# Kernel optimization log

Measured on AMD Instinct MI355X. Metric: run time of the kernel, lower is better.

## Reference

```python
import jax, jax.numpy as jnp
import numpy as np

B, T, IN_DIM, HID, OUT_DIM = 32, 2000, 118, 256, 118


def sru_layer(x, W, b):
    """One SRU layer. x: [B,T,n_in]; W: [n_in, k*d] with k=3 (n_in==d) or k=4; b: [2*d].
    c_t = f_t*c_{t-1} + (1-f_t)*x~_t ;  h_t = r_t*tanh(c_t) + (1-r_t)*x_hw_t
    """
    d = b.shape[0] // 2
    k = W.shape[1] // d
    U = jnp.einsum('bti,io->bto', x, W)  # [B,T,k*d] gate precompute (GEMM)
    x_tilde = U[..., :d]
    f = jax.nn.sigmoid(U[..., d:2 * d] + b[:d])
    r = jax.nn.sigmoid(U[..., 2 * d:3 * d] + b[d:])
    x_hw = U[..., 3 * d:4 * d] if k == 4 else x  # highway input (projected if dims differ)

    # elementwise recurrent scan over time (time-major)
    def step(c, ft_xt):
        ft, xt = ft_xt
        c = ft * c + (1.0 - ft) * xt
        return c, c

    f_t = jnp.swapaxes(f, 0, 1)        # [T,B,d]
    x_t = jnp.swapaxes(x_tilde, 0, 1)  # [T,B,d]
    c0 = jnp.zeros((x.shape[0], d), dtype=x.dtype)
    _, c_seq = jax.lax.scan(step, c0, (f_t, x_t))
    c = jnp.swapaxes(c_seq, 0, 1)      # [B,T,d]
    return r * jnp.tanh(c) + (1.0 - r) * x_hw


def setup_inputs() -> dict:
    key = jax.random.key(0)
    ks = jax.random.split(key, 8)
    sequence = jax.random.normal(ks[0], (B, T, IN_DIM), dtype=jnp.float32)
    lengths = jax.random.randint(ks[1], (B,), 1, T + 1)
    s0 = 1.0 / np.sqrt(IN_DIM)
    s1 = 1.0 / np.sqrt(HID)
    W0 = jax.random.uniform(ks[2], (IN_DIM, 4 * HID), jnp.float32, -s0, s0)  # k=4: n_in != n_out
    b0 = jnp.zeros((2 * HID,), jnp.float32)
    W1 = jax.random.uniform(ks[3], (HID, 3 * HID), jnp.float32, -s1, s1)    # k=3: n_in == n_out
    b1 = jnp.zeros((2 * HID,), jnp.float32)
    Wout = jax.random.uniform(ks[4], (HID, OUT_DIM), jnp.float32, -s1, s1)
    bout = jax.random.uniform(ks[5], (OUT_DIM,), jnp.float32, -s1, s1)
    return {"sequence": sequence, "lengths": lengths, "W0": W0, "b0": b0,
            "W1": W1, "b1": b1, "Wout": Wout, "bout": bout}


def reference(sequence, lengths, W0, b0, W1, b1, Wout, bout):
    h = sru_layer(sequence, W0, b0)
    h = sru_layer(h, W1, b1)
    out = jnp.einsum('btd,do->bto', h, Wout) + bout  # hidden2out Linear
    return out  # last_sigmoid=False
```

## Files before the change

kernel.cpp:

```cpp
#include <hip/hip_runtime.h>


typedef __attribute__((ext_vector_type(8))) __bf16 bf16x8;
typedef __attribute__((ext_vector_type(4))) float f32x4;
typedef __attribute__((ext_vector_type(4))) unsigned int u32x4;

static __device__ __forceinline__ float fast_sigmoid(float x) {
    float e = __expf(-x);
    return __builtin_amdgcn_rcpf(1.f + e);
}
static __device__ __forceinline__ float fast_tanh(float x) {
    float e = __expf(-2.f * fabsf(x));
    float t = (1.f - e) * __builtin_amdgcn_rcpf(1.f + e);
    return copysignf(t, x);
}
static __device__ __forceinline__ unsigned short f2bf(float f) {
    union { float f; unsigned u; } v; v.f = f;
    return (unsigned short)((v.u + 0x7fffu + ((v.u >> 16) & 1u)) >> 16);
}
static __device__ __forceinline__ float bf2f(unsigned short h) {
    union { unsigned u; float f; } v; v.u = ((unsigned)h) << 16;
    return v.f;
}

static constexpr int T = 2000;

__global__ void prep_x_kernel(const float* __restrict__ x, unsigned short* __restrict__ xp) {
    int i = blockIdx.x * 256 + threadIdx.x;
    if (i >= 64000 * 128) return;
    int row = i >> 7, k = i & 127;
    float v = (k < 118) ? x[row * 118 + k] : 0.f;
    xp[i] = f2bf(v);
}

__global__ void prep_w_kernel(const float* __restrict__ W0, const float* __restrict__ W1,
                              const float* __restrict__ Wout,
                              unsigned short* __restrict__ W0t, unsigned short* __restrict__ W1t,
                              unsigned short* __restrict__ Wot) {
    int i = blockIdx.x * 256 + threadIdx.x;
    if (i < 1024 * 128) {
        int n = i >> 7, k = i & 127;
        float v = (k < 118) ? W0[k * 1024 + n] : 0.f;
        W0t[i] = f2bf(v);
        return;
    }
    i -= 1024 * 128;
    if (i < 768 * 256) {
        int n = i >> 8, k = i & 255;
        W1t[i] = f2bf(W1[k * 768 + n]);
        return;
    }
    i -= 768 * 256;
    if (i < 128 * 256) {
        int n = i >> 8, k = i & 255;
        float v = (n < 118) ? Wout[k * 118 + n] : 0.f;
        Wot[i] = f2bf(v);
    }
}

template <int KP, int KFAC>
__global__ __launch_bounds__(256, 4)
void sru_wave_kernel(const unsigned short* __restrict__ xin,
                     const unsigned short* __restrict__ Wt,
                     const float* __restrict__ bvec,
                     unsigned short* __restrict__ hout) {
    constexpr int KST   = KP / 32;
    constexpr int CPR   = KP / 8;
    constexpr int ROWB  = KP * 2;
    constexpr int CHUNK = 250;
    constexpr int WARM  = 64;

    __shared__ unsigned short sW[KFAC * 16 * KP];

    const int tid   = threadIdx.x;
    const int lane  = tid & 63;
    const int w     = tid >> 6;
    const int slice = blockIdx.x >> 6;
    const int chunk = (blockIdx.x >> 3) & 7;
    const int bgrp  = blockIdx.x & 7;
    const int d0    = slice * 16;
    const int b     = bgrp * 4 + w;

    {
        constexpr int NCHK = KFAC * 16 * CPR;
        for (int i = tid; i < NCHK; i += 256) {
            int row = i / CPR, c = i % CPR;
            int ch = row & 15, gate = row >> 4;
            u32x4 v = *(const u32x4*)(Wt + (size_t)(gate * 256 + d0 + ch) * KP + c * 8);
            *(u32x4*)((char*)sW + row * ROWB + ((c * 16) ^ (ch << 4))) = v;
        }
    }
    __syncthreads();

    const int nl = lane & 15;
    const int q  = lane >> 4;

    const float bf_r = bvec[d0 + nl];
    const float br_r = bvec[256 + d0 + nl];

    const unsigned short* xb = xin + (size_t)b * T * KP;
    unsigned short* hb = hout + (size_t)b * T * 256;

    const int tR = chunk * CHUNK;
    const int tW = chunk ? tR - WARM : 0;
    const int tE = tR + CHUNK;

    float c_in = 0.f;

    for (int t0 = tW; t0 < tE; t0 += 16) {
        int ta = t0 + nl; if (ta > T - 1) ta = T - 1;
        const unsigned short* ap = xb + (size_t)ta * KP + q * 8;

        unsigned short xh[4];
        if constexpr (KFAC == 3) {
#pragma unroll
            for (int j = 0; j < 4; ++j) {
                int t = t0 + q * 4 + j;
                if (t > T - 1) t = T - 1;
                xh[j] = xb[(size_t)t * KP + d0 + nl];
            }
        }

        f32x4 acc[KFAC];
        const f32x4 fz = {0.f, 0.f, 0.f, 0.f};
#pragma unroll
        for (int g = 0; g < KFAC; ++g) acc[g] = fz;
        const char* sWb = (const char*)sW;
        const int swz = nl << 4;
#pragma unroll
        for (int ks = 0; ks < KST; ++ks) {
            bf16x8 a = *(const bf16x8*)(ap + ks * 32);
            const int koff = (ks * 64 + q * 16) ^ swz;
#pragma unroll
            for (int g = 0; g < KFAC; ++g) {
                bf16x8 bb = *(const bf16x8*)(sWb + (g * 16 + nl) * ROWB + koff);
                acc[g] = __builtin_amdgcn_mfma_f32_16x16x32_bf16(a, bb, acc[g], 0, 0, 0);
            }
        }

        f32x4 fv, gv, rv;
#pragma unroll
        for (int j = 0; j < 4; ++j) {
            float f = fast_sigmoid(acc[1][j] + bf_r);
            fv[j] = f;
            gv[j] = (1.f - f) * acc[0][j];
            rv[j] = fast_sigmoid(acc[2][j] + br_r);
        }

        float F = fv[0] * fv[1];
        float G = gv[0];
        G = __builtin_fmaf(fv[1], G, gv[1]);
        G = __builtin_fmaf(fv[2], G, gv[2]);
        G = __builtin_fmaf(fv[3], G, gv[3]);
        F = F * fv[2] * fv[3];

        float Pf = 1.f, Pg = 0.f, Sf = F, Sg = G;
#pragma unroll
        for (int d = 16; d <= 32; d <<= 1) {
            float of = __shfl_xor(Sf, d);
            float og = __shfl_xor(Sg, d);
            const bool later = (lane & d) != 0;
            if (later) { Pg = __builtin_fmaf(Pf, og, Pg); Pf *= of; }
            float nSg = later ? __builtin_fmaf(Sf, og, Sg)
                              : __builtin_fmaf(of, Sg, og);
            Sf = Sf * of;
            Sg = nSg;
        }

        float cc = __builtin_fmaf(Pf, c_in, Pg);
#pragma unroll
        for (int j = 0; j < 4; ++j) {
            cc = __builtin_fmaf(fv[j], cc, gv[j]);
            int t = t0 + q * 4 + j;
            if (t >= tR && t < tE) {
                float xhw;
                if constexpr (KFAC == 4)
                    xhw = acc[3][j];
                else
                    xhw = bf2f(xh[j]);
                float h = rv[j] * fast_tanh(cc) + (1.f - rv[j]) * xhw;
                hb[(size_t)t * 256 + d0 + nl] = f2bf(h);
            }
        }
        c_in = __builtin_fmaf(Sf, c_in, Sg);
    }
}

__global__ __launch_bounds__(256, 2)
void out_gemm_kernel(const unsigned short* __restrict__ h1,
                     const unsigned short* __restrict__ Wt,
                     const float* __restrict__ bout,
                     float* __restrict__ out) {
    constexpr int K = 256, LDA = 264;
    const int tid = threadIdx.x, lane = tid & 63, w = tid >> 6;
    const int m0 = (blockIdx.x >> 1) * 64;
    const int n0 = (blockIdx.x & 1) * 64;

    __shared__ unsigned short sA[64 * LDA];

    bf16x8 bfrag[4][8];
    {
        const int nl = lane & 15, kq = (lane >> 4) * 8;
#pragma unroll
        for (int nt = 0; nt < 4; ++nt) {
            const unsigned short* src = Wt + (n0 + nt * 16 + nl) * K + kq;
#pragma unroll
            for (int ks = 0; ks < 8; ++ks)
                bfrag[nt][ks] = *(const bf16x8*)(src + ks * 32);
        }
    }
    {
#pragma unroll
        for (int base = 0; base < 2048; base += 256) {
            int idx = base + tid;
            int r = idx >> 5, cc = idx & 31;
            *(u32x4*)&sA[r * LDA + cc * 8] = *(const u32x4*)(h1 + (size_t)(m0 + r) * K + cc * 8);
        }
    }
    __syncthreads();

    f32x4 acc[4];
    f32x4 fz = {0.f, 0.f, 0.f, 0.f};
#pragma unroll
    for (int nt = 0; nt < 4; ++nt) acc[nt] = fz;
    {
        const unsigned short* arow = &sA[(16 * w + (lane & 15)) * LDA + (lane >> 4) * 8];
#pragma unroll
        for (int ks = 0; ks < 8; ++ks) {
            bf16x8 a = *(const bf16x8*)(arow + ks * 32);
#pragma unroll
            for (int nt = 0; nt < 4; ++nt)
                acc[nt] = __builtin_amdgcn_mfma_f32_16x16x32_bf16(a, bfrag[nt][ks], acc[nt], 0, 0, 0);
        }
    }
    {
        const int nl = lane & 15;
        const int rbase = m0 + 16 * w + (lane >> 4) * 4;
#pragma unroll
        for (int nt = 0; nt < 4; ++nt) {
            int col = n0 + nt * 16 + nl;
            if (col < 118) {
                float bo = bout[col];
#pragma unroll
                for (int j = 0; j < 4; ++j)
                    out[(size_t)(rbase + j) * 118 + col] = acc[nt][j] + bo;
            }
        }
    }
}

extern "C" void kernel_launch(void* const* d_in, const int* in_sizes, int n_in,
                              void* d_out, int out_size, void* d_ws, size_t ws_size,
                              hipStream_t stream) {
    const float* seq  = (const float*)d_in[0];
    const float* W0   = (const float*)d_in[2];
    const float* b0   = (const float*)d_in[3];
    const float* W1   = (const float*)d_in[4];
    const float* b1   = (const float*)d_in[5];
    const float* Wout = (const float*)d_in[6];
    const float* bout = (const float*)d_in[7];
    float* out = (float*)d_out;

    char* ws = (char*)d_ws;
    size_t off = 0;
    auto alloc = [&](size_t bytes) -> void* {
        void* p = ws + off;
        off = (off + bytes + 255) & ~(size_t)255;
        return p;
    };
    unsigned short* x0p = (unsigned short*)alloc(64000ull * 128 * 2);
    unsigned short* h0b = (unsigned short*)alloc(64000ull * 256 * 2);
    unsigned short* h1b = (unsigned short*)alloc(64000ull * 256 * 2);
    unsigned short* W0t = (unsigned short*)alloc(1024ull * 128 * 2);
    unsigned short* W1t = (unsigned short*)alloc(768ull * 256 * 2);
    unsigned short* Wot = (unsigned short*)alloc(128ull * 256 * 2);
    if (ws_size < off) return;

    prep_x_kernel<<<dim3(32000), dim3(256), 0, stream>>>(seq, x0p);
    prep_w_kernel<<<dim3(1408), dim3(256), 0, stream>>>(W0, W1, Wout, W0t, W1t, Wot);
    sru_wave_kernel<128, 4><<<dim3(1024), dim3(256), 0, stream>>>(x0p, W0t, b0, h0b);
    sru_wave_kernel<256, 3><<<dim3(1024), dim3(256), 0, stream>>>(h0b, W1t, b1, h1b);
    out_gemm_kernel<<<dim3(2000), dim3(256), 0, stream>>>(h1b, Wot, bout, out);
}
```

Baseline: 202.3 us.

## Use time-contiguous k-blocked layout for SRU inputs and prefetch next A tile

The padded input and the layer-0 hidden output are stored in a [B][K/8][T][8] layout, so each MFMA A-fragment load of 16 consecutive timesteps reads one contiguous 256-byte span instead of rows strided by the full K width. The layer-1 highway read and the layer-0 output write are remapped to match, while layer-1 still writes the linear layout used by the output GEMM. The A fragments for the next 16-step block are loaded right after the current MFMAs to hide global latency behind the gate and scan math. The cost is more live registers and scattered 2-byte writes in the prep and layer-0 store paths.

Result: slower. 239.4 us (+18.3%).

```diff
diff --git a/kernel.cpp b/kernel.cpp
--- a/kernel.cpp
+++ b/kernel.cpp
@@ -30,7 +30,10 @@
     if (i >= 64000 * 128) return;
     int row = i >> 7, k = i & 127;
     float v = (k < 118) ? x[row * 118 + k] : 0.f;
-    xp[i] = f2bf(v);
+    int b = row / 2000;
+    int t = row - b * 2000;
+    size_t idx = (((size_t)b * 16 + (k >> 3)) * 2000 + t) * 8 + (k & 7);
+    xp[idx] = f2bf(v);
 }
 
 __global__ void prep_w_kernel(const float* __restrict__ W0, const float* __restrict__ W1,
@@ -58,7 +61,7 @@
     }
 }
 
-template <int KP, int KFAC>
+template <int KP, int KFAC, bool OTR>
 __global__ __launch_bounds__(256, 4)
 void sru_wave_kernel(const unsigned short* __restrict__ xin,
                      const unsigned short* __restrict__ Wt,
@@ -99,25 +102,40 @@
     const float br_r = bvec[256 + d0 + nl];
 
     const unsigned short* xb = xin + (size_t)b * T * KP;
-    unsigned short* hb = hout + (size_t)b * T * 256;
-
     const int tR = chunk * CHUNK;
     const int tW = chunk ? tR - WARM : 0;
     const int tE = tR + CHUNK;
 
+    unsigned short* hb_lin = hout + (size_t)b * T * 256;
+    unsigned short* hb_tr  = hout + ((size_t)b * 32 + ((d0 + nl) >> 3)) * T * 8
+                                   + ((d0 + nl) & 7);
+
+    const unsigned short* xh_base = xb + (size_t)((d0 + nl) >> 3) * T * 8 + ((d0 + nl) & 7);
+
     float c_in = 0.f;
 
+    const char* sWb = (const char*)sW;
+    const int swz = nl << 4;
+
+    auto aload = [&](int t0, bf16x8* a) {
+        int ta = t0 + nl; if (ta > T - 1) ta = T - 1;
+        const unsigned short* ap = xb + ((size_t)q * T + ta) * 8;
+#pragma unroll
+        for (int ks = 0; ks < KST; ++ks)
+            a[ks] = *(const bf16x8*)(ap + (size_t)ks * 4 * T * 8);
+    };
+
+    bf16x8 aC[KST];
+    aload(tW, aC);
+
     for (int t0 = tW; t0 < tE; t0 += 16) {
-        int ta = t0 + nl; if (ta > T - 1) ta = T - 1;
-        const unsigned short* ap = xb + (size_t)ta * KP + q * 8;
-
         unsigned short xh[4];
         if constexpr (KFAC == 3) {
 #pragma unroll
             for (int j = 0; j < 4; ++j) {
                 int t = t0 + q * 4 + j;
                 if (t > T - 1) t = T - 1;
-                xh[j] = xb[(size_t)t * KP + d0 + nl];
+                xh[j] = xh_base[(size_t)t * 8];
             }
         }
 
@@ -125,18 +143,17 @@
         const f32x4 fz = {0.f, 0.f, 0.f, 0.f};
 #pragma unroll
         for (int g = 0; g < KFAC; ++g) acc[g] = fz;
-        const char* sWb = (const char*)sW;
-        const int swz = nl << 4;
 #pragma unroll
         for (int ks = 0; ks < KST; ++ks) {
-            bf16x8 a = *(const bf16x8*)(ap + ks * 32);
             const int koff = (ks * 64 + q * 16) ^ swz;
 #pragma unroll
             for (int g = 0; g < KFAC; ++g) {
                 bf16x8 bb = *(const bf16x8*)(sWb + (g * 16 + nl) * ROWB + koff);
-                acc[g] = __builtin_amdgcn_mfma_f32_16x16x32_bf16(a, bb, acc[g], 0, 0, 0);
+                acc[g] = __builtin_amdgcn_mfma_f32_16x16x32_bf16(aC[ks], bb, acc[g], 0, 0, 0);
             }
         }
+
+        aload(t0 + 16, aC);
 
         f32x4 fv, gv, rv;
 #pragma unroll
@@ -179,7 +196,10 @@
                 else
                     xhw = bf2f(xh[j]);
                 float h = rv[j] * fast_tanh(cc) + (1.f - rv[j]) * xhw;
-                hb[(size_t)t * 256 + d0 + nl] = f2bf(h);
+                if constexpr (OTR)
+                    hb_tr[(size_t)t * 8] = f2bf(h);
+                else
+                    hb_lin[(size_t)t * 256 + d0 + nl] = f2bf(h);
             }
         }
         c_in = __builtin_fmaf(Sf, c_in, Sg);
@@ -278,7 +298,7 @@
 
     prep_x_kernel<<<dim3(32000), dim3(256), 0, stream>>>(seq, x0p);
     prep_w_kernel<<<dim3(1408), dim3(256), 0, stream>>>(W0, W1, Wout, W0t, W1t, Wot);
-    sru_wave_kernel<128, 4><<<dim3(1024), dim3(256), 0, stream>>>(x0p, W0t, b0, h0b);
-    sru_wave_kernel<256, 3><<<dim3(1024), dim3(256), 0, stream>>>(h0b, W1t, b1, h1b);
+    sru_wave_kernel<128, 4, true ><<<dim3(1024), dim3(256), 0, stream>>>(x0p, W0t, b0, h0b);
+    sru_wave_kernel<256, 3, false><<<dim3(1024), dim3(256), 0, stream>>>(h0b, W1t, b1, h1b);
     out_gemm_kernel<<<dim3(2000), dim3(256), 0, stream>>>(h1b, Wot, bout, out);
 }
```
